# Optimization experiments

Hardware: AMD Instinct MI355X
Metric: run time of the kernel (lower is better)

Reference implementation:

```python
import jax, jax.numpy as jnp
import numpy as np

D_MODEL = 1024
NUM_HEADS = 16
D_K = D_MODEL // NUM_HEADS
D_FF = 4096
B, S = 16, 512


def setup_inputs() -> dict:
    key = jax.random.key(0)
    ks = jax.random.split(key, 9)
    scale = 1.0 / np.sqrt(D_MODEL)
    inp = {
        "x": jax.random.normal(ks[0], (B, S, D_MODEL), dtype=jnp.float32),
        # attention projections, stored as [in, out] (apply as x @ W)
        "Wq": jax.random.normal(ks[1], (D_MODEL, D_MODEL), dtype=jnp.float32) * scale,
        "Wk": jax.random.normal(ks[2], (D_MODEL, D_MODEL), dtype=jnp.float32) * scale,
        "Wv": jax.random.normal(ks[3], (D_MODEL, D_MODEL), dtype=jnp.float32) * scale,
        "Wo": jax.random.normal(ks[4], (D_MODEL, D_MODEL), dtype=jnp.float32) * scale,
        # FFN
        "W1": jax.random.normal(ks[5], (D_MODEL, D_FF), dtype=jnp.float32) * scale,
        "b1": jnp.zeros((D_FF,), dtype=jnp.float32),
        "W2": jax.random.normal(ks[6], (D_FF, D_MODEL), dtype=jnp.float32) * (1.0 / np.sqrt(D_FF)),
        "b2": jnp.zeros((D_MODEL,), dtype=jnp.float32),
        # LayerNorms
        "g1": jnp.ones((D_MODEL,), dtype=jnp.float32),
        "be1": jnp.zeros((D_MODEL,), dtype=jnp.float32),
        "g2": jnp.ones((D_MODEL,), dtype=jnp.float32),
        "be2": jnp.zeros((D_MODEL,), dtype=jnp.float32),
    }
    return inp


def _layernorm(x, g, b, eps=1e-5):
    mu = jnp.mean(x, axis=-1, keepdims=True)
    var = jnp.mean(jnp.square(x - mu), axis=-1, keepdims=True)
    return (x - mu) * jax.lax.rsqrt(var + eps) * g + b


def _mha(x, Wq, Wk, Wv, Wo):
    b, s, _ = x.shape
    def split(h):  # [b,s,d] -> [b,H,s,dk]
        return h.reshape(b, s, NUM_HEADS, D_K).transpose(0, 2, 1, 3)
    Q, K, V = split(x @ Wq), split(x @ Wk), split(x @ Wv)
    scores = jnp.einsum("bhqd,bhkd->bhqk", Q, K) / np.sqrt(D_K)  # [b,H,s,s]
    causal = jnp.triu(jnp.ones((s, s), dtype=bool), k=1)
    scores = jnp.where(causal, -jnp.inf, scores)
    weights = jax.nn.softmax(scores, axis=-1)
    attn = jnp.einsum("bhqk,bhkd->bhqd", weights, V)
    attn = attn.transpose(0, 2, 1, 3).reshape(b, s, D_MODEL)
    return attn @ Wo


def reference(x, Wq, Wk, Wv, Wo, W1, b1, W2, b2, g1, be1, g2, be2):
    # pre-norm transformer block, dropout = 0 (eval)
    x = x + _mha(_layernorm(x, g1, be1), Wq, Wk, Wv, Wo)
    h = _layernorm(x, g2, be2)
    ffn = jax.nn.relu(h @ W1 + b1) @ W2 + b2
    return x + ffn
```

## Files before the change

kernel.cpp:

```cpp
#include <hip/hip_runtime.h>
#include <stdint.h>

#define NH 16
#define DK 64
#define BB 16
#define SS 512
#define DM 1024
#define DFF 4096

typedef __attribute__((ext_vector_type(8))) __bf16 bf16x8;
typedef __attribute__((ext_vector_type(4))) float  float4v;

__device__ __forceinline__ unsigned short f2bf(float f) {
  union { float f; unsigned int u; } v; v.f = f;
  unsigned int u = v.u + 0x7fffu + ((v.u >> 16) & 1u);
  return (unsigned short)(u >> 16);
}

__device__ __forceinline__ void gld_lds16(const void* g, void* l) {
  __builtin_amdgcn_global_load_lds(
      (const __attribute__((address_space(1))) unsigned int*)g,
      (__attribute__((address_space(3))) unsigned int*)l, 16, 0, 0);
}

__global__ void transpose_all(const float* __restrict__ Wq, const float* __restrict__ Wk,
                              const float* __restrict__ Wv, const float* __restrict__ Wo,
                              const float* __restrict__ W1, const float* __restrict__ W2,
                              unsigned short* __restrict__ WqkvT, unsigned short* __restrict__ WoT,
                              unsigned short* __restrict__ W1T, unsigned short* __restrict__ W2T) {
  __shared__ float tile[32][33];
  int bid = blockIdx.x;
  const float* in; unsigned short* out; int R, C, tl;
  if (bid < 1024)      { in = Wq; out = WqkvT;            R = 1024; C = 1024; tl = bid; }
  else if (bid < 2048) { in = Wk; out = WqkvT + 1048576;  R = 1024; C = 1024; tl = bid - 1024; }
  else if (bid < 3072) { in = Wv; out = WqkvT + 2097152;  R = 1024; C = 1024; tl = bid - 2048; }
  else if (bid < 4096) { in = Wo; out = WoT;              R = 1024; C = 1024; tl = bid - 3072; }
  else if (bid < 8192) { in = W1; out = W1T;              R = 1024; C = 4096; tl = bid - 4096; }
  else                 { in = W2; out = W2T;              R = 4096; C = 1024; tl = bid - 8192; }
  int ntx = C >> 5;
  int c0 = (tl % ntx) * 32, r0 = (tl / ntx) * 32;
  int tx = threadIdx.x, ty = threadIdx.y;
  for (int j = ty; j < 32; j += 8)
    tile[j][tx] = in[(size_t)(r0 + j) * C + c0 + tx];
  __syncthreads();
  for (int j = ty; j < 32; j += 8)
    out[(size_t)(c0 + j) * R + r0 + tx] = f2bf(tile[tx][j]);
}

__global__ __launch_bounds__(256) void ln_bf16(const float* __restrict__ in,
                                               const float* __restrict__ g,
                                               const float* __restrict__ be,
                                               unsigned short* __restrict__ out) {
  int row = blockIdx.x, t = threadIdx.x;
  const float4* in4 = (const float4*)(in + (size_t)row * DM);
  float4 v = in4[t];
  float s  = v.x + v.y + v.z + v.w;
  float s2 = v.x * v.x + v.y * v.y + v.z * v.z + v.w * v.w;
  for (int off = 1; off < 64; off <<= 1) { s += __shfl_xor(s, off); s2 += __shfl_xor(s2, off); }
  __shared__ float rs[4], rs2[4];
  int wave = t >> 6;
  if ((t & 63) == 0) { rs[wave] = s; rs2[wave] = s2; }
  __syncthreads();
  s  = rs[0] + rs[1] + rs[2] + rs[3];
  s2 = rs2[0] + rs2[1] + rs2[2] + rs2[3];
  float mu = s * (1.f / DM);
  float var = s2 * (1.f / DM) - mu * mu;
  float rstd = rsqrtf(var + 1e-5f);
  float4 gv = ((const float4*)g)[t];
  float4 bv = ((const float4*)be)[t];
  unsigned short o0 = f2bf((v.x - mu) * rstd * gv.x + bv.x);
  unsigned short o1 = f2bf((v.y - mu) * rstd * gv.y + bv.y);
  unsigned short o2 = f2bf((v.z - mu) * rstd * gv.z + bv.z);
  unsigned short o3 = f2bf((v.w - mu) * rstd * gv.w + bv.w);
  uint2 pk; pk.x = o0 | ((unsigned)o1 << 16); pk.y = o2 | ((unsigned)o3 << 16);
  *(uint2*)(out + (size_t)row * DM + t * 4) = pk;
}

template <int MODE>
__global__ __launch_bounds__(256, 2)
void gemm_bt(const unsigned short* __restrict__ A, const unsigned short* __restrict__ Bt,
             int M, int N, int K,
             const float* __restrict__ bias, const float* __restrict__ resid,
             float* __restrict__ outf, unsigned short* __restrict__ outb,
             unsigned short* __restrict__ qo, unsigned short* __restrict__ ko,
             unsigned short* __restrict__ vo) {
  __shared__ __align__(16) unsigned short As[128 * 32];
  __shared__ __align__(16) unsigned short Bs[128 * 32];
  const int t = threadIdx.x, lane = t & 63, wave = t >> 6;
  const int lc = lane & 15, lr = lane >> 4;
  const int wm = wave >> 1, wn = wave & 1;

  const int nbn = gridDim.x;
  int pid = blockIdx.y * nbn + blockIdx.x;
  int nig = nbn << 3;
  int gid = pid / nig;
  int loc = pid - gid * nig;
  const int rowblk = (gid * 8 + (loc & 7)) * 128;
  const int colblk = (loc >> 3) * 128;

  float4v acc[4][4];
#pragma unroll
  for (int i = 0; i < 4; i++)
#pragma unroll
    for (int j = 0; j < 4; j++) acc[i][j] = (float4v)0.f;

  const int r0 = t >> 2;
  const int sg = ((t & 3) ^ ((r0 >> 1) & 3));
  const int ldsoff = r0 * 32 + (t & 3) * 8;
  const int goff = sg * 8;

  for (int k0 = 0; k0 < K; k0 += 32) {
#pragma unroll
    for (int c = 0; c < 2; c++) {
      int row = c * 64 + r0;
      gld_lds16(A  + (size_t)(rowblk + row) * K + k0 + goff, &As[c * 2048 + ldsoff]);
      gld_lds16(Bt + (size_t)(colblk + row) * K + k0 + goff, &Bs[c * 2048 + ldsoff]);
    }
    __syncthreads();
    bf16x8 af[4], bfr[4];
    const int slot = (lr ^ ((lc >> 1) & 3)) * 8;
#pragma unroll
    for (int mt = 0; mt < 4; mt++)
      af[mt] = *(const bf16x8*)&As[(wm * 64 + mt * 16 + lc) * 32 + slot];
#pragma unroll
    for (int nt = 0; nt < 4; nt++)
      bfr[nt] = *(const bf16x8*)&Bs[(wn * 64 + nt * 16 + lc) * 32 + slot];
#pragma unroll
    for (int mt = 0; mt < 4; mt++)
#pragma unroll
      for (int nt = 0; nt < 4; nt++)
        acc[mt][nt] = __builtin_amdgcn_mfma_f32_16x16x32_bf16(af[mt], bfr[nt], acc[mt][nt], 0, 0, 0);
    __syncthreads();
  }

#pragma unroll
  for (int mt = 0; mt < 4; mt++)
#pragma unroll
    for (int nt = 0; nt < 4; nt++)
#pragma unroll
      for (int r = 0; r < 4; r++) {
        int row = rowblk + wm * 64 + mt * 16 + lr * 4 + r;
        int col = colblk + wn * 64 + nt * 16 + lc;
        float v = acc[mt][nt][r];
        if (MODE == 0) {
          int b = row >> 9, s = row & 511;
          int f = col & 1023, h = f >> 6, d = f & 63;
          if (col < 1024)
            qo[(((size_t)b * NH + h) * SS + s) * DK + d] = f2bf(v);
          else if (col < 2048)
            ko[(((size_t)b * NH + h) * SS + s) * DK + d] = f2bf(v);
          else
            vo[(((size_t)b * NH + h) * DK + d) * SS + s] = f2bf(v);
        } else if (MODE == 1) {
          outf[(size_t)row * N + col] = resid[(size_t)row * N + col] + v;
        } else if (MODE == 2) {
          outb[(size_t)row * N + col] = f2bf(fmaxf(v + bias[col], 0.f));
        } else {
          outf[(size_t)row * N + col] = resid[(size_t)row * N + col] + v + bias[col];
        }
      }
}

__global__ __launch_bounds__(256, 2)
void attn(const unsigned short* __restrict__ Qb, const unsigned short* __restrict__ Kb,
          const unsigned short* __restrict__ Vtb, unsigned short* __restrict__ Ob) {
  __shared__ __align__(16) unsigned short Qs[128 * 64];
  __shared__ __align__(16) unsigned short Ks[128 * 64];
  __shared__ __align__(16) unsigned short Vts[64 * 128];
  __shared__ __align__(16) unsigned short Ps[4 * 32 * 128];
  const int t = threadIdx.x, lane = t & 63, wave = t >> 6;
  const int lc = lane & 15, lr = lane >> 4;
  const int qt = blockIdx.x, h = blockIdx.y, b = blockIdx.z;
  const int Q0 = qt * 128;
  const size_t headQK = ((size_t)b * NH + h) * SS * DK;
  const size_t headV  = ((size_t)b * NH + h) * DK * SS;
  const float SCALE = 0.125f, L2E = 1.44269504f;

  const int qkg = ((t & 7) ^ ((t >> 3) & 7)) * 8;
  const int qkrow = (t >> 3) * 64;
  const int vg = ((t & 15) ^ ((t >> 4) & 7)) * 8;
  const int vrow = t >> 4;

  {
    const unsigned short* gq = Qb + headQK + (size_t)Q0 * DK;
#pragma unroll
    for (int c = 0; c < 4; c++)
      gld_lds16(gq + c * 2048 + qkrow + qkg, &Qs[c * 2048 + t * 8]);
  }

  float4v o_acc[2][4];
#pragma unroll
  for (int mt = 0; mt < 2; mt++)
#pragma unroll
    for (int nt = 0; nt < 4; nt++) o_acc[mt][nt] = (float4v)0.f;
  float m_i[2][4], l_i[2][4];
#pragma unroll
  for (int mt = 0; mt < 2; mt++)
#pragma unroll
    for (int r = 0; r < 4; r++) { m_i[mt][r] = -__builtin_inff(); l_i[mt][r] = 0.f; }

  for (int kt = 0; kt <= qt; kt++) {
    __syncthreads();
    const unsigned short* gk = Kb + headQK + (size_t)kt * 128 * DK;
#pragma unroll
    for (int c = 0; c < 4; c++)
      gld_lds16(gk + c * 2048 + qkrow + qkg, &Ks[c * 2048 + t * 8]);
#pragma unroll
    for (int c = 0; c < 4; c++) {
      int d = c * 16 + vrow;
      gld_lds16(Vtb + headV + (size_t)d * SS + kt * 128 + vg, &Vts[c * 2048 + t * 8]);
    }
    __syncthreads();

    float4v s[2][8];
#pragma unroll
    for (int mt = 0; mt < 2; mt++)
#pragma unroll
      for (int nt = 0; nt < 8; nt++) s[mt][nt] = (float4v)0.f;
#pragma unroll
    for (int kk = 0; kk < 2; kk++) {
      bf16x8 aq[2];
#pragma unroll
      for (int mt = 0; mt < 2; mt++) {
        int row = wave * 32 + mt * 16 + lc;
        aq[mt] = *(const bf16x8*)&Qs[row * 64 + (((kk * 4 + lr) ^ (lc & 7)) * 8)];
      }
#pragma unroll
      for (int nt = 0; nt < 8; nt++) {
        int row = nt * 16 + lc;
        bf16x8 bk = *(const bf16x8*)&Ks[row * 64 + (((kk * 4 + lr) ^ (lc & 7)) * 8)];
#pragma unroll
        for (int mt = 0; mt < 2; mt++)
          s[mt][nt] = __builtin_amdgcn_mfma_f32_16x16x32_bf16(aq[mt], bk, s[mt][nt], 0, 0, 0);
      }
    }
    const bool diag = (kt == qt);
#pragma unroll
    for (int mt = 0; mt < 2; mt++)
#pragma unroll
      for (int nt = 0; nt < 8; nt++)
#pragma unroll
        for (int r = 0; r < 4; r++) {
          float sv = s[mt][nt][r] * SCALE;
          if (diag && (nt * 16 + lc > wave * 32 + mt * 16 + lr * 4 + r)) sv = -__builtin_inff();
          s[mt][nt][r] = sv;
        }
    float alpha_a[2][4];
#pragma unroll
    for (int mt = 0; mt < 2; mt++)
#pragma unroll
      for (int r = 0; r < 4; r++) {
        float mx = -__builtin_inff();
#pragma unroll
        for (int nt = 0; nt < 8; nt++) mx = fmaxf(mx, s[mt][nt][r]);
        for (int off = 1; off < 16; off <<= 1) mx = fmaxf(mx, __shfl_xor(mx, off));
        float mnew = fmaxf(m_i[mt][r], mx);
        float alpha = exp2f((m_i[mt][r] - mnew) * L2E);
        m_i[mt][r] = mnew;
        float rsum = 0.f;
#pragma unroll
        for (int nt = 0; nt < 8; nt++) {
          float p = exp2f((s[mt][nt][r] - mnew) * L2E);
          s[mt][nt][r] = p;
          rsum += p;
        }
        for (int off = 1; off < 16; off <<= 1) rsum += __shfl_xor(rsum, off);
        l_i[mt][r] = l_i[mt][r] * alpha + rsum;
        alpha_a[mt][r] = alpha;
      }
#pragma unroll
    for (int mt = 0; mt < 2; mt++)
#pragma unroll
      for (int nt = 0; nt < 4; nt++)
#pragma unroll
        for (int r = 0; r < 4; r++) o_acc[mt][nt][r] *= alpha_a[mt][r];
    const int wbase = wave * 32 * 128;
#pragma unroll
    for (int mt = 0; mt < 2; mt++)
#pragma unroll
      for (int nt = 0; nt < 8; nt++) {
        int g = nt * 2 + (lc >> 3);
#pragma unroll
        for (int r = 0; r < 4; r++) {
          int rowp = mt * 16 + lr * 4 + r;
          Ps[wbase + rowp * 128 + ((g ^ (rowp & 7)) * 8) + (lc & 7)] = f2bf(s[mt][nt][r]);
        }
      }
#pragma unroll
    for (int kk = 0; kk < 4; kk++) {
      bf16x8 ap[2];
#pragma unroll
      for (int mt = 0; mt < 2; mt++) {
        int rowp = mt * 16 + lc;
        ap[mt] = *(const bf16x8*)&Ps[wbase + rowp * 128 + (((kk * 4 + lr) ^ (lc & 7)) * 8)];
      }
#pragma unroll
      for (int nt = 0; nt < 4; nt++) {
        int row = nt * 16 + lc;
        bf16x8 bv = *(const bf16x8*)&Vts[row * 128 + (((kk * 4 + lr) ^ (lc & 7)) * 8)];
#pragma unroll
        for (int mt = 0; mt < 2; mt++)
          o_acc[mt][nt] = __builtin_amdgcn_mfma_f32_16x16x32_bf16(ap[mt], bv, o_acc[mt][nt], 0, 0, 0);
      }
    }
  }
  float inv[2][4];
#pragma unroll
  for (int mt = 0; mt < 2; mt++)
#pragma unroll
    for (int r = 0; r < 4; r++) inv[mt][r] = 1.f / l_i[mt][r];
#pragma unroll
  for (int mt = 0; mt < 2; mt++)
#pragma unroll
    for (int nt = 0; nt < 4; nt++)
#pragma unroll
      for (int r = 0; r < 4; r++) {
        int sg = Q0 + wave * 32 + mt * 16 + lr * 4 + r;
        int col = h * DK + nt * 16 + lc;
        Ob[((size_t)b * SS + sg) * DM + col] = f2bf(o_acc[mt][nt][r] * inv[mt][r]);
      }
}

extern "C" void kernel_launch(void* const* d_in, const int* in_sizes, int n_in,
                              void* d_out, int out_size, void* d_ws, size_t ws_size,
                              hipStream_t stream) {
  const float* x  = (const float*)d_in[0];
  const float* Wq = (const float*)d_in[1];
  const float* Wk = (const float*)d_in[2];
  const float* Wv = (const float*)d_in[3];
  const float* Wo = (const float*)d_in[4];
  const float* W1 = (const float*)d_in[5];
  const float* b1 = (const float*)d_in[6];
  const float* W2 = (const float*)d_in[7];
  const float* b2 = (const float*)d_in[8];
  const float* g1 = (const float*)d_in[9];
  const float* be1 = (const float*)d_in[10];
  const float* g2 = (const float*)d_in[11];
  const float* be2 = (const float*)d_in[12];

  char* ws = (char*)d_ws;
  unsigned short* WqkvT = (unsigned short*)(ws);
  unsigned short* WoT   = (unsigned short*)(ws + 6291456);
  unsigned short* W1T   = (unsigned short*)(ws + 8388608);
  unsigned short* W2T   = (unsigned short*)(ws + 16777216);
  unsigned short* hbuf  = (unsigned short*)(ws + 25165824);
  unsigned short* Qb    = (unsigned short*)(ws + 41943040);
  unsigned short* Kb    = (unsigned short*)(ws + 58720256);
  unsigned short* Vtb   = (unsigned short*)(ws + 75497472);
  unsigned short* attnO = (unsigned short*)(ws + 92274688);
  float*          x1    = (float*)(ws + 109051904);
  unsigned short* ffn1  = (unsigned short*)(ws + 41943040);

  transpose_all<<<12288, dim3(32, 8), 0, stream>>>(Wq, Wk, Wv, Wo, W1, W2,
                                                   WqkvT, WoT, W1T, W2T);

  ln_bf16<<<8192, 256, 0, stream>>>(x, g1, be1, hbuf);

  gemm_bt<0><<<dim3(24, 64), 256, 0, stream>>>(hbuf, WqkvT, 8192, 3072, 1024,
      nullptr, nullptr, nullptr, nullptr, Qb, Kb, Vtb);

  attn<<<dim3(4, NH, BB), 256, 0, stream>>>(Qb, Kb, Vtb, attnO);

  gemm_bt<1><<<dim3(8, 64), 256, 0, stream>>>(attnO, WoT, 8192, 1024, 1024,
      nullptr, x, x1, nullptr, nullptr, nullptr, nullptr);

  ln_bf16<<<8192, 256, 0, stream>>>(x1, g2, be2, hbuf);

  gemm_bt<2><<<dim3(32, 64), 256, 0, stream>>>(hbuf, W1T, 8192, 4096, 1024,
      b1, nullptr, nullptr, ffn1, nullptr, nullptr, nullptr);

  gemm_bt<3><<<dim3(8, 64), 256, 0, stream>>>(ffn1, W2T, 8192, 1024, 4096,
      b2, x1, (float*)d_out, nullptr, nullptr, nullptr, nullptr);
}
```

Before: 504.1 us.

## Split-K the output-projection and FFN2 GEMMs with atomic accumulation

Adds a split-K template parameter to the GEMM and runs the Wo and W2 projections with two K-slices per tile. Partial results are accumulated with float atomicAdd into outputs zeroed by memsets, and only the first slice adds the residual and bias. The intent is more blocks in flight for the N=1024 GEMMs. In exchange it adds two large memsets and atomic read-modify-write traffic on the outputs.

```diff
diff --git a/kernel.cpp b/kernel.cpp
--- a/kernel.cpp
+++ b/kernel.cpp
@@ -76,7 +76,7 @@
   *(uint2*)(out + (size_t)row * DM + t * 4) = pk;
 }
 
-template <int MODE>
+template <int MODE, int SPLITK>
 __global__ __launch_bounds__(256, 2)
 void gemm_bt(const unsigned short* __restrict__ A, const unsigned short* __restrict__ Bt,
              int M, int N, int K,
@@ -109,12 +109,14 @@
   const int ldsoff = r0 * 32 + (t & 3) * 8;
   const int goff = sg * 8;
 
-  for (int k0 = 0; k0 < K; k0 += 32) {
+  const int kbeg = (SPLITK > 1) ? blockIdx.z * (K / SPLITK) : 0;
+  const int kend = kbeg + K / SPLITK;
+
+  for (int k0 = kbeg; k0 < kend; k0 += 32) {
 #pragma unroll
     for (int c = 0; c < 2; c++) {
-      int row = c * 64 + r0;
-      gld_lds16(A  + (size_t)(rowblk + row) * K + k0 + goff, &As[c * 2048 + ldsoff]);
-      gld_lds16(Bt + (size_t)(colblk + row) * K + k0 + goff, &Bs[c * 2048 + ldsoff]);
+      gld_lds16(A  + (size_t)(rowblk + c * 64 + r0) * K + k0 + goff, &As[c * 2048 + ldsoff]);
+      gld_lds16(Bt + (size_t)(colblk + c * 64 + r0) * K + k0 + goff, &Bs[c * 2048 + ldsoff]);
     }
     __syncthreads();
     bf16x8 af[4], bfr[4];
@@ -133,6 +135,7 @@
     __syncthreads();
   }
 
+  const bool lead = (SPLITK == 1) || (blockIdx.z == 0);
 #pragma unroll
   for (int mt = 0; mt < 4; mt++)
 #pragma unroll
@@ -152,11 +155,15 @@
           else
             vo[(((size_t)b * NH + h) * DK + d) * SS + s] = f2bf(v);
         } else if (MODE == 1) {
-          outf[(size_t)row * N + col] = resid[(size_t)row * N + col] + v;
+          float add = v;
+          if (lead) add += resid[(size_t)row * N + col];
+          atomicAdd(&outf[(size_t)row * N + col], add);
         } else if (MODE == 2) {
           outb[(size_t)row * N + col] = f2bf(fmaxf(v + bias[col], 0.f));
         } else {
-          outf[(size_t)row * N + col] = resid[(size_t)row * N + col] + v + bias[col];
+          float add = v;
+          if (lead) add += resid[(size_t)row * N + col] + bias[col];
+          atomicAdd(&outf[(size_t)row * N + col], add);
         }
       }
 }
@@ -315,9 +322,9 @@
     for (int nt = 0; nt < 4; nt++)
 #pragma unroll
       for (int r = 0; r < 4; r++) {
-        int sg = Q0 + wave * 32 + mt * 16 + lr * 4 + r;
+        int sg2 = Q0 + wave * 32 + mt * 16 + lr * 4 + r;
         int col = h * DK + nt * 16 + lc;
-        Ob[((size_t)b * SS + sg) * DM + col] = f2bf(o_acc[mt][nt][r] * inv[mt][r]);
+        Ob[((size_t)b * SS + sg2) * DM + col] = f2bf(o_acc[mt][nt][r] * inv[mt][r]);
       }
 }
 
@@ -351,24 +358,27 @@
   float*          x1    = (float*)(ws + 109051904);
   unsigned short* ffn1  = (unsigned short*)(ws + 41943040);
 
+  hipMemsetAsync(x1, 0, 33554432, stream);
+  hipMemsetAsync(d_out, 0, 33554432, stream);
+
   transpose_all<<<12288, dim3(32, 8), 0, stream>>>(Wq, Wk, Wv, Wo, W1, W2,
                                                    WqkvT, WoT, W1T, W2T);
 
   ln_bf16<<<8192, 256, 0, stream>>>(x, g1, be1, hbuf);
 
-  gemm_bt<0><<<dim3(24, 64), 256, 0, stream>>>(hbuf, WqkvT, 8192, 3072, 1024,
+  gemm_bt<0, 1><<<dim3(24, 64), 256, 0, stream>>>(hbuf, WqkvT, 8192, 3072, 1024,
       nullptr, nullptr, nullptr, nullptr, Qb, Kb, Vtb);
 
   attn<<<dim3(4, NH, BB), 256, 0, stream>>>(Qb, Kb, Vtb, attnO);
 
-  gemm_bt<1><<<dim3(8, 64), 256, 0, stream>>>(attnO, WoT, 8192, 1024, 1024,
+  gemm_bt<1, 2><<<dim3(8, 64, 2), 256, 0, stream>>>(attnO, WoT, 8192, 1024, 1024,
       nullptr, x, x1, nullptr, nullptr, nullptr, nullptr);
 
   ln_bf16<<<8192, 256, 0, stream>>>(x1, g2, be2, hbuf);
 
-  gemm_bt<2><<<dim3(32, 64), 256, 0, stream>>>(hbuf, W1T, 8192, 4096, 1024,
+  gemm_bt<2, 1><<<dim3(32, 64), 256, 0, stream>>>(hbuf, W1T, 8192, 4096, 1024,
       b1, nullptr, nullptr, ffn1, nullptr, nullptr, nullptr);
 
-  gemm_bt<3><<<dim3(8, 64), 256, 0, stream>>>(ffn1, W2T, 8192, 1024, 4096,
+  gemm_bt<3, 2><<<dim3(8, 64, 2), 256, 0, stream>>>(ffn1, W2T, 8192, 1024, 4096,
       b2, x1, (float*)d_out, nullptr, nullptr, nullptr, nullptr);
 }
```

Result: slower. 592.3 us (+17.5%).
